# Kernel optimization log

Measured on AMD Instinct MI355X. Metric: run time of the kernel, lower is better.

Reference implementation:

```python
import jax, jax.numpy as jnp
import numpy as np

H = 256          # NUM_HIDDEN_NODES
D = 2 * H        # encoder feature dim
C_CLS = 1000     # NUM_CLASSES
B = 16
S = 1024
STEPS = 8
WINDOW = 4
MIN_VAL = 1e-8   # min_val global in original


def moving_sum(x, back, fwd):
    # x: [B, T]; sum over window [i-back, i+fwd] (zero padded), as conv1d with ones kernel
    xp = jnp.pad(x, ((0, 0), (back, fwd)))
    k = jnp.ones((1, 1, back + fwd + 1), x.dtype)
    y = jax.lax.conv_general_dilated(xp[:, None, :], k, window_strides=(1,),
                                     padding='VALID', dimension_numbers=('NCH', 'OIH', 'NCH'))
    return y[:, 0, :]


def setup_inputs() -> dict:
    key = jax.random.key(0)
    ks = jax.random.split(key, 24)
    def lin(k, i, o):
        return jax.random.normal(k, (i, o), jnp.float32) * np.float32(1.0 / np.sqrt(i))
    def vec(k, n):
        return jax.random.normal(k, (n,), jnp.float32) * np.float32(1.0 / np.sqrt(n))
    return {
        'enc_output': jax.random.normal(ks[0], (B, S, D), jnp.float32),
        'target': jax.random.randint(ks[1], (B, STEPS), 0, C_CLS),
        'length_enc': jax.random.randint(ks[2], (B,), S // 2, S + 1),
        'noise': jax.random.normal(ks[3], (STEPS, B, S), jnp.float32),
        'Ws_mono_w': lin(ks[4], H, D), 'Ws_mono_b': jnp.zeros((D,), jnp.float32),
        'Wh_mono': lin(ks[5], D, D),
        'v_mono': vec(ks[6], D),
        'g_mono': jnp.full((1,), 1.0 / np.sqrt(D), jnp.float32),
        'r_mono': jnp.full((1,), -4.0, jnp.float32),
        'Ws_chunk_w': lin(ks[7], H, D), 'Ws_chunk_b': jnp.zeros((D,), jnp.float32),
        'Wh_chunk': lin(ks[8], D, D),
        'v_chunk': vec(ks[9], D),
        'L_sy': lin(ks[10], H, H),
        'L_gy_w': lin(ks[11], D, H), 'L_gy_b': jnp.zeros((H,), jnp.float32),
        'L_yy_w': lin(ks[12], H, C_CLS), 'L_yy_b': jnp.zeros((C_CLS,), jnp.float32),
        'L_ys': jax.random.normal(ks[13], (C_CLS, 4 * H), jnp.float32) * 0.02,
        'L_ss': lin(ks[14], H, 4 * H),
        'L_gs_w': lin(ks[15], D, 4 * H), 'L_gs_b': jnp.zeros((4 * H,), jnp.float32),
    }


def reference(enc_output, target, length_enc, noise,
              Ws_mono_w, Ws_mono_b, Wh_mono, v_mono, g_mono, r_mono,
              Ws_chunk_w, Ws_chunk_b, Wh_chunk, v_chunk,
              L_sy, L_gy_w, L_gy_b, L_yy_w, L_yy_b, L_ys, L_ss, L_gs_w, L_gs_b):
    Bn, Sn, _ = enc_output.shape
    Hn = L_sy.shape[0]
    mask = jnp.arange(Sn)[None, :] >= length_enc[:, None]   # True = padded
    neg_inf = jnp.float32(-jnp.inf)
    # step-invariant encoder projections (hoisted out of decode loop)
    enc_mono = enc_output @ Wh_mono     # [B,S,D]
    enc_chunk = enc_output @ Wh_chunk   # [B,S,D]
    v_norm = g_mono[0] / jnp.linalg.norm(v_mono)

    def step(carry, xs):
        s, c, a_prev = carry
        nz, tgt = xs
        # monotonic energies
        tmp1 = jnp.tanh(enc_mono + (s @ Ws_mono_w + Ws_mono_b)[:, None, :])
        e_mono = jnp.einsum('bsd,d->bs', v_norm * tmp1, v_mono) + r_mono[0]
        e_mono = jnp.where(mask, neg_inf, e_mono)
        p = jax.nn.sigmoid(e_mono + nz)
        # monotonic attention recurrence via stable cumsum/cumprod
        logf = jnp.log(jnp.clip(1.0 - p[:, :-1], MIN_VAL, 1.0))
        cpp = jnp.concatenate([jnp.ones((Bn, 1), p.dtype), jnp.exp(jnp.cumsum(logf, axis=1))], axis=1)
        q = cpp * jnp.cumsum(a_prev / jnp.clip(cpp, MIN_VAL, 1.0), axis=1)
        alpha = jnp.clip(p * q, MIN_VAL, 1.0)
        # chunkwise attention
        tmp2 = jnp.tanh(enc_chunk + (s @ Ws_chunk_w + Ws_chunk_b)[:, None, :])
        e_ch = jnp.where(mask, neg_inf, jnp.einsum('bsd,d->bs', tmp2, v_chunk))
        e_ch = e_ch - jnp.max(e_ch, axis=1, keepdims=True)
        ex = jnp.clip(jnp.exp(e_ch), 1e-5, None)
        denom = jnp.clip(moving_sum(ex, WINDOW - 1, 0), 1e-10, None)
        beta = ex * moving_sum(alpha / denom, 0, WINDOW - 1)
        ctx = jnp.einsum('bs,bsd->bd', beta, enc_output)
        # decoder LSTM cell
        rec = L_ys[tgt] + s @ L_ss + ctx @ L_gs_w + L_gs_b
        i, f, g, o = jnp.split(rec, 4, axis=1)
        c_new = jax.nn.sigmoid(f) * c + jax.nn.sigmoid(i) * jnp.tanh(g)
        s_new = jax.nn.sigmoid(o) * jnp.tanh(c_new)
        y = jnp.tanh(ctx @ L_gy_w + L_gy_b + s_new @ L_sy) @ L_yy_w + L_yy_b
        return (s_new, c_new, jax.lax.stop_gradient(alpha)), y

    a0 = jnp.zeros((Bn, Sn), enc_output.dtype).at[:, 0].set(1.0)
    s0 = jnp.zeros((Bn, Hn), enc_output.dtype)
    c0 = jnp.zeros((Bn, Hn), enc_output.dtype)
    _, ys = jax.lax.scan(step, (s0, c0, a0), (noise, target.T))
    return jnp.transpose(ys, (1, 0, 2))   # [B, steps, NUM_CLASSES]
```

## Files before the change

kernel.cpp:

```cpp
#include <hip/hip_runtime.h>
#include <math.h>
#include <float.h>

#define HN 256
#define DN 512
#define CCLS 1000
#define BB 16
#define SS 1024
#define NSTEPS 8
#define G4 1024
#define KV 768

using f16x8 = __attribute__((ext_vector_type(8))) _Float16;
using f32x4 = __attribute__((ext_vector_type(4))) float;

__device__ __forceinline__ void gload_lds16(const void* g, void* l) {
    __builtin_amdgcn_global_load_lds((const __attribute__((address_space(1))) void*)g,
                                     (__attribute__((address_space(3))) void*)l, 16, 0, 0);
}

__device__ __forceinline__ float ftanh(float x) {
    float e = __expf(2.f * x);
    return 1.f - 2.f / (e + 1.f);
}
__device__ __forceinline__ float fsigm(float x) {
    return 1.f / (1.f + __expf(-x));
}

__global__ __launch_bounds__(512) void init_k(const float* __restrict__ vM, const float* __restrict__ g,
                                              const float* __restrict__ Wsmb, const float* __restrict__ Wscb,
                                              float* __restrict__ aA, float* __restrict__ sA,
                                              float* __restrict__ cbuf,
                                              float* __restrict__ smb, float* __restrict__ scb,
                                              float* __restrict__ vn) {
    int bid = blockIdx.x, t = threadIdx.x;
    if (bid == 80) {
        __shared__ float red[512];
        float x = vM[t];
        red[t] = x * x;
        __syncthreads();
        for (int off = 256; off > 0; off >>= 1) {
            if (t < off) red[t] += red[t + off];
            __syncthreads();
        }
        if (t == 0) vn[0] = g[0] / sqrtf(red[0]);
        return;
    }
    int i = bid * 512 + t;
    if (i < 16384) {
        aA[i] = ((i & (SS - 1)) == 0) ? 1.f : 0.f;
    } else if (i < 20480) {
        sA[i - 16384] = 0.f;
    } else if (i < 24576) {
        cbuf[i - 20480] = 0.f;
    } else if (i < 32768) {
        int j = i - 24576;
        smb[j] = Wsmb[j & (DN - 1)];
    } else {
        int j = i - 32768;
        scb[j] = Wscb[j & (DN - 1)];
    }
}

__global__ __launch_bounds__(256) void conv_enc_k(const float* __restrict__ in,
                                                  _Float16* __restrict__ out) {
    size_t i = ((size_t)blockIdx.x * 256 + threadIdx.x) * 8;
    float4 a = *(const float4*)(in + i);
    float4 b = *(const float4*)(in + i + 4);
    f16x8 o;
    o[0] = (_Float16)a.x; o[1] = (_Float16)a.y; o[2] = (_Float16)a.z; o[3] = (_Float16)a.w;
    o[4] = (_Float16)b.x; o[5] = (_Float16)b.y; o[6] = (_Float16)b.z; o[7] = (_Float16)b.w;
    *(f16x8*)(out + i) = o;
}

__global__ __launch_bounds__(256) void convW_k(const float* __restrict__ W1,
                                               const float* __restrict__ W2,
                                               _Float16* __restrict__ WcT) {
    int kt = blockIdx.x;
    int nt = blockIdx.y;
    __shared__ _Float16 tile[32][33];
    int tx = threadIdx.x & 31, ty = threadIdx.x >> 5;
    int n0 = nt * 32, k0 = kt * 32;
    for (int r = 0; r < 32; r += 8) {
        int k = k0 + ty + r, n = n0 + tx;
        float v = (n < 512) ? W1[(size_t)k * 512 + n] : W2[(size_t)k * 512 + (n - 512)];
        tile[tx][ty + r] = (_Float16)v;
    }
    __syncthreads();
    for (int r = 0; r < 32; r += 8) {
        int n = n0 + ty + r, k = k0 + tx;
        WcT[(size_t)n * 512 + k] = tile[ty + r][tx];
    }
}

__global__ __launch_bounds__(256) void transAll_k(const float* __restrict__ Lss, const float* __restrict__ Lgs,
                                                  const float* __restrict__ Lsy, const float* __restrict__ Lgy,
                                                  const float* __restrict__ Wsm, const float* __restrict__ Wsc,
                                                  const float* __restrict__ Lyy,
                                                  float* __restrict__ WgT, float* __restrict__ WyT,
                                                  float* __restrict__ WpT, float* __restrict__ LyyT) {
    int bid = blockIdx.x;
    const float* src; float* dst; int R, C, dstride, coloff, ctiles;
    if (bid < 256)       { src = Lss; dst = WgT;  R = 256; C = 1024; dstride = KV; coloff = 0;  ctiles = 32; }
    else if (bid < 768)  { src = Lgs; dst = WgT;  R = 512; C = 1024; dstride = KV; coloff = HN; ctiles = 32; bid -= 256; }
    else if (bid < 832)  { src = Lsy; dst = WyT;  R = 256; C = 256;  dstride = KV; coloff = 0;  ctiles = 8;  bid -= 768; }
    else if (bid < 960)  { src = Lgy; dst = WyT;  R = 512; C = 256;  dstride = KV; coloff = HN; ctiles = 8;  bid -= 832; }
    else if (bid < 1088) { src = Wsm; dst = WpT;  R = 256; C = 512;  dstride = HN; coloff = 0;  ctiles = 16; bid -= 960; }
    else if (bid < 1216) { src = Wsc; dst = WpT + (size_t)DN * HN; R = 256; C = 512; dstride = HN; coloff = 0; ctiles = 16; bid -= 1088; }
    else                 { src = Lyy; dst = LyyT; R = 256; C = 1000; dstride = HN; coloff = 0;  ctiles = 32; bid -= 1216; }
    int ct = bid % ctiles, rt = bid / ctiles;
    __shared__ float tile[32][33];
    int c0 = ct * 32, r0 = rt * 32;
    int tx = threadIdx.x & 31, ty = threadIdx.x >> 5;
    for (int rr = 0; rr < 32; rr += 8) {
        int r = r0 + ty + rr, cc = c0 + tx;
        tile[ty + rr][tx] = (r < R && cc < C) ? src[(size_t)r * C + cc] : 0.f;
    }
    __syncthreads();
    for (int rr = 0; rr < 32; rr += 8) {
        int cc = c0 + ty + rr, r = r0 + tx;
        if (cc < C && r < R) dst[(size_t)cc * dstride + coloff + r] = tile[tx][ty + rr];
    }
}

__global__ __launch_bounds__(256) void gemm16_k(const _Float16* __restrict__ A16,
                                                const _Float16* __restrict__ WcT,
                                                _Float16* __restrict__ encMC) {
    __shared__ _Float16 Alds[128 * 32];
    __shared__ _Float16 Blds[128 * 32];
    int bm = blockIdx.x;
    int bn = blockIdx.y;
    int tid = threadIdx.x;
    int lane = tid & 63;
    int w = tid >> 6;
    int wr = w >> 1, wc = w & 1;
    int lr = lane & 15;
    int kg = lane >> 4;
    f32x4 acc[4][4];
#pragma unroll
    for (int i = 0; i < 4; i++)
#pragma unroll
        for (int j = 0; j < 4; j++) acc[i][j] = (f32x4){0.f, 0.f, 0.f, 0.f};
    int wavebase = tid & ~63;
    for (int k0 = 0; k0 < 512; k0 += 32) {
        __syncthreads();
#pragma unroll
        for (int is = 0; is < 2; is++) {
            int l = is * 256 + tid;
            int row = l >> 2, kgs = l & 3;
            int kp = kgs ^ ((row ^ (row >> 2)) & 3);
            gload_lds16(A16 + (size_t)(bm * 128 + row) * 512 + k0 + kp * 8,
                        (char*)Alds + (size_t)(is * 256 + wavebase) * 16);
            gload_lds16(WcT + (size_t)(bn * 128 + row) * 512 + k0 + kp * 8,
                        (char*)Blds + (size_t)(is * 256 + wavebase) * 16);
        }
        __syncthreads();
        f16x8 af[4], bf[4];
#pragma unroll
        for (int mi = 0; mi < 4; mi++) {
            int r = wr * 64 + mi * 16 + lr;
            int kp = kg ^ ((r ^ (r >> 2)) & 3);
            af[mi] = *(const f16x8*)(Alds + r * 32 + kp * 8);
        }
#pragma unroll
        for (int ni = 0; ni < 4; ni++) {
            int cgl = wc * 64 + ni * 16 + lr;
            int kp = kg ^ ((cgl ^ (cgl >> 2)) & 3);
            bf[ni] = *(const f16x8*)(Blds + cgl * 32 + kp * 8);
        }
#pragma unroll
        for (int mi = 0; mi < 4; mi++)
#pragma unroll
            for (int ni = 0; ni < 4; ni++)
                acc[mi][ni] = __builtin_amdgcn_mfma_f32_16x16x32_f16(af[mi], bf[ni], acc[mi][ni], 0, 0, 0);
    }
    int cr = lane >> 4;
#pragma unroll
    for (int mi = 0; mi < 4; mi++)
#pragma unroll
        for (int ni = 0; ni < 4; ni++) {
            int col = bn * 128 + wc * 64 + ni * 16 + lr;
#pragma unroll
            for (int j = 0; j < 4; j++) {
                int row = bm * 128 + wr * 64 + mi * 16 + cr * 4 + j;
                encMC[(size_t)row * 1024 + col] = (_Float16)acc[mi][ni][j];
            }
        }
}

__device__ __forceinline__ void out_proj(int bid2, int tid, float* shbuf,
                                         const float* __restrict__ yv,
                                         const float* __restrict__ LyyT, const float* __restrict__ Lyyb,
                                         float* __restrict__ out, int tt) {
    for (int i = tid * 4; i < BB * HN; i += 1024)
        *(float4*)&shbuf[i] = *(const float4*)&yv[i];
    __syncthreads();
    int wave = tid >> 6, lane = tid & 63;
    int c0 = (bid2 * 4 + wave) * 4;
    for (int q = 0; q < 4; q++) {
        int cc = c0 + q;
        if (cc >= CCLS) break;
        const float* wp = LyyT + (size_t)cc * HN;
        float acc[BB] = {0.f};
#pragma unroll
        for (int k = 0; k < 4; k++) {
            int e = lane + k * 64;
            float wv = wp[e];
#pragma unroll
            for (int b = 0; b < BB; b++) acc[b] = fmaf(wv, shbuf[b * HN + e], acc[b]);
        }
#pragma unroll
        for (int b = 0; b < BB; b++)
#pragma unroll
            for (int off = 32; off > 0; off >>= 1) acc[b] += __shfl_xor(acc[b], off);
        if (lane == 0) {
            float bias = Lyyb[cc];
#pragma unroll
            for (int b = 0; b < BB; b++) out[((size_t)b * NSTEPS + tt) * CCLS + cc] = acc[b] + bias;
        }
    }
}

__global__ __launch_bounds__(256) void energy_out_k(const _Float16* __restrict__ encMC,
                                                    const float* __restrict__ sm, const float* __restrict__ sc,
                                                    const float* __restrict__ vM, const float* __restrict__ vC,
                                                    const float* __restrict__ vnorm, const float* __restrict__ rmono,
                                                    const int* __restrict__ len, const float* __restrict__ noise_t,
                                                    float* __restrict__ p, float* __restrict__ ech,
                                                    const float* __restrict__ yv,
                                                    const float* __restrict__ LyyT, const float* __restrict__ Lyyb,
                                                    float* __restrict__ out, int t) {
    __shared__ float shbuf[BB * HN];
    int tid = threadIdx.x;
    if (blockIdx.x >= 4096) {
        if (t > 0) out_proj(blockIdx.x - 4096, tid, shbuf, yv, LyyT, Lyyb, out, t - 1);
        return;
    }
    int wave = blockIdx.x * 4 + (tid >> 6);
    int lane = tid & 63;
    int b = wave >> 10;
    int si = wave & 1023;
    const f16x8* row = (const f16x8*)(encMC + (size_t)wave * 1024);
    f16x8 em = row[lane];
    f16x8 ec = row[64 + lane];
    int d0 = lane * 8;
    float4 sma = *(const float4*)&sm[b * DN + d0];
    float4 smbv = *(const float4*)&sm[b * DN + d0 + 4];
    float4 sca = *(const float4*)&sc[b * DN + d0];
    float4 scbv = *(const float4*)&sc[b * DN + d0 + 4];
    float4 vma = *(const float4*)&vM[d0];
    float4 vmb = *(const float4*)&vM[d0 + 4];
    float4 vca = *(const float4*)&vC[d0];
    float4 vcb = *(const float4*)&vC[d0 + 4];
    float smv[8] = {sma.x, sma.y, sma.z, sma.w, smbv.x, smbv.y, smbv.z, smbv.w};
    float scv[8] = {sca.x, sca.y, sca.z, sca.w, scbv.x, scbv.y, scbv.z, scbv.w};
    float vmv[8] = {vma.x, vma.y, vma.z, vma.w, vmb.x, vmb.y, vmb.z, vmb.w};
    float vcv[8] = {vca.x, vca.y, vca.z, vca.w, vcb.x, vcb.y, vcb.z, vcb.w};
    float s1 = 0.f, s2 = 0.f;
#pragma unroll
    for (int j = 0; j < 8; j++) {
        s1 += ftanh((float)em[j] + smv[j]) * vmv[j];
        s2 += ftanh((float)ec[j] + scv[j]) * vcv[j];
    }
#pragma unroll
    for (int off = 32; off > 0; off >>= 1) {
        s1 += __shfl_xor(s1, off);
        s2 += __shfl_xor(s2, off);
    }
    if (lane == 0) {
        bool masked = (si >= len[b]);
        float pe = 0.f;
        if (!masked) pe = fsigm(vnorm[0] * s1 + rmono[0] + noise_t[b * SS + si]);
        p[b * SS + si] = pe;
        ech[b * SS + si] = masked ? -INFINITY : s2;
    }
}

__global__ __launch_bounds__(64) void scan_k(const float* __restrict__ p,
                                             const float* __restrict__ aprev,
                                             const float* __restrict__ ech,
                                             float* __restrict__ anew,
                                             float* __restrict__ beta) {
    int b = blockIdx.x;
    int l = threadIdx.x;
    int base = b * SS + l * 16;
    float pv[16], ap[16], eh[16];
#pragma unroll
    for (int k = 0; k < 16; k += 4) {
        *(float4*)&pv[k] = *(const float4*)&p[base + k];
        *(float4*)&ap[k] = *(const float4*)&aprev[base + k];
        *(float4*)&eh[k] = *(const float4*)&ech[base + k];
    }
    float ls[16];
    float run = 0.f;
#pragma unroll
    for (int k = 0; k < 16; k++) {
        float lf = __logf(fminf(fmaxf(1.f - pv[k], 1e-8f), 1.f));
        if (l == 63 && k == 15) lf = 0.f;
        run += lf;
        ls[k] = run;
    }
    float incl = run;
#pragma unroll
    for (int off = 1; off < 64; off <<= 1) {
        float n = __shfl_up(incl, off);
        if (l >= off) incl += n;
    }
    float basew = incl - run;
    float cpp[16];
#pragma unroll
    for (int k = 0; k < 16; k++)
        cpp[k] = __expf(basew + (k ? ls[k - 1] : 0.f));
    float us[16];
    float run2 = 0.f;
#pragma unroll
    for (int k = 0; k < 16; k++) {
        run2 += ap[k] / fminf(fmaxf(cpp[k], 1e-8f), 1.f);
        us[k] = run2;
    }
    float incl2 = run2;
#pragma unroll
    for (int off = 1; off < 64; off <<= 1) {
        float n = __shfl_up(incl2, off);
        if (l >= off) incl2 += n;
    }
    float basew2 = incl2 - run2;
    float al[16];
#pragma unroll
    for (int k = 0; k < 16; k++)
        al[k] = fminf(fmaxf(pv[k] * (cpp[k] * (basew2 + us[k])), 1e-8f), 1.f);
#pragma unroll
    for (int k = 0; k < 16; k += 4)
        *(float4*)&anew[base + k] = *(float4*)&al[k];
    float mx = eh[0];
#pragma unroll
    for (int k = 1; k < 16; k++) mx = fmaxf(mx, eh[k]);
#pragma unroll
    for (int off = 32; off > 0; off >>= 1) mx = fmaxf(mx, __shfl_xor(mx, off));
    float ex[16];
#pragma unroll
    for (int k = 0; k < 16; k++) ex[k] = fmaxf(__expf(eh[k] - mx), 1e-5f);
    float exm1 = __shfl_up(ex[15], 1); if (l == 0) exm1 = 0.f;
    float exm2 = __shfl_up(ex[14], 1); if (l == 0) exm2 = 0.f;
    float exm3 = __shfl_up(ex[13], 1); if (l == 0) exm3 = 0.f;
    float r[16];
    {
        float d0 = ex[0] + exm1 + exm2 + exm3;
        float d1 = ex[1] + ex[0] + exm1 + exm2;
        float d2 = ex[2] + ex[1] + ex[0] + exm1;
        r[0] = al[0] / fmaxf(d0, 1e-10f);
        r[1] = al[1] / fmaxf(d1, 1e-10f);
        r[2] = al[2] / fmaxf(d2, 1e-10f);
    }
#pragma unroll
    for (int k = 3; k < 16; k++)
        r[k] = al[k] / fmaxf(ex[k] + ex[k - 1] + ex[k - 2] + ex[k - 3], 1e-10f);
    float rp1 = __shfl_down(r[0], 1); if (l == 63) rp1 = 0.f;
    float rp2 = __shfl_down(r[1], 1); if (l == 63) rp2 = 0.f;
    float rp3 = __shfl_down(r[2], 1); if (l == 63) rp3 = 0.f;
    float bt[16];
#pragma unroll
    for (int k = 0; k < 13; k++)
        bt[k] = ex[k] * (r[k] + r[k + 1] + r[k + 2] + r[k + 3]);
    bt[13] = ex[13] * (r[13] + r[14] + r[15] + rp1);
    bt[14] = ex[14] * (r[14] + r[15] + rp1 + rp2);
    bt[15] = ex[15] * (r[15] + rp1 + rp2 + rp3);
#pragma unroll
    for (int k = 0; k < 16; k += 4)
        *(float4*)&beta[base + k] = *(float4*)&bt[k];
}

__global__ __launch_bounds__(512) void ctxpart_k(const float* __restrict__ beta,
                                                 const _Float16* __restrict__ enc16,
                                                 float* __restrict__ part8) {
    __shared__ float red[8][DN];
    int b = blockIdx.x, ch = blockIdx.y;
    int tid = threadIdx.x, wv = tid >> 6, lane = tid & 63;
    int s0 = ch * 128;
    float acc[8] = {0.f};
    const _Float16* ebase = enc16 + ((size_t)(b * SS + s0)) * DN + lane * 8;
    const float* bp = beta + b * SS + s0;
#pragma unroll 4
    for (int rr = 0; rr < 16; rr++) {
        int s = wv + rr * 8;
        float bv = bp[s];
        f16x8 ld = *(const f16x8*)(ebase + (size_t)s * DN);
#pragma unroll
        for (int j = 0; j < 8; j++) acc[j] = fmaf(bv, (float)ld[j], acc[j]);
    }
#pragma unroll
    for (int j = 0; j < 8; j++) red[wv][lane * 8 + j] = acc[j];
    __syncthreads();
    float s = 0.f;
#pragma unroll
    for (int wq = 0; wq < 8; wq++) s += red[wq][tid];
    part8[((size_t)(b * 8 + ch)) * DN + tid] = s;
}

__global__ __launch_bounds__(512) void gl_k(const float* __restrict__ part8,
                                            const float* __restrict__ sIn,
                                            const float* __restrict__ WgT,
                                            const int* __restrict__ target, int t,
                                            const float* __restrict__ Lys, const float* __restrict__ Lgsb,
                                            float* __restrict__ c, float* __restrict__ sOut,
                                            float* __restrict__ ctxbuf) {
    __shared__ float xl[BB * KV];
    __shared__ float recL[16][BB];
    int tid = threadIdx.x;
    for (int i = tid; i < BB * HN; i += 512)
        xl[(i >> 8) * KV + (i & (HN - 1))] = sIn[i];
    for (int i = tid; i < BB * DN; i += 512) {
        int bb = i >> 9, d = i & (DN - 1);
        const float* pp = part8 + (size_t)bb * (8 * DN) + d;
        float v = ((pp[0] + pp[DN]) + (pp[2 * DN] + pp[3 * DN])) +
                  ((pp[4 * DN] + pp[5 * DN]) + (pp[6 * DN] + pp[7 * DN]));
        xl[bb * KV + HN + d] = v;
        if (blockIdx.x == 0) ctxbuf[i] = v;
    }
    __syncthreads();
    int wv = tid >> 6, lane = tid & 63;
    int h0 = blockIdx.x * 4;
    int ri0 = wv * 2, ri1 = ri0 + 1;
    const float* w0p = WgT + (size_t)((ri0 >> 2) * HN + h0 + (ri0 & 3)) * KV;
    const float* w1p = WgT + (size_t)((ri1 >> 2) * HN + h0 + (ri1 & 3)) * KV;
    float acc0[BB] = {0.f}, acc1[BB] = {0.f};
#pragma unroll
    for (int j = 0; j < 12; j++) {
        int e = lane + j * 64;
        float w0 = w0p[e], w1 = w1p[e];
#pragma unroll
        for (int b = 0; b < BB; b++) {
            float xv = xl[b * KV + e];
            acc0[b] = fmaf(w0, xv, acc0[b]);
            acc1[b] = fmaf(w1, xv, acc1[b]);
        }
    }
#pragma unroll
    for (int b = 0; b < BB; b++)
#pragma unroll
        for (int off = 32; off > 0; off >>= 1) {
            acc0[b] += __shfl_xor(acc0[b], off);
            acc1[b] += __shfl_xor(acc1[b], off);
        }
    if (lane == 0) {
#pragma unroll
        for (int b = 0; b < BB; b++) {
            recL[ri0][b] = acc0[b];
            recL[ri1][b] = acc1[b];
        }
    }
    __syncthreads();
    if (tid < 64) {
        int b = tid & 15, hh = tid >> 4;
        int h = h0 + hh;
        int tgt = target[b * NSTEPS + t];
        const float* ys = Lys + (size_t)tgt * G4;
        float ri = recL[0 * 4 + hh][b] + ys[h] + Lgsb[h];
        float rf = recL[1 * 4 + hh][b] + ys[h + HN] + Lgsb[h + HN];
        float rg = recL[2 * 4 + hh][b] + ys[h + 2 * HN] + Lgsb[h + 2 * HN];
        float ro = recL[3 * 4 + hh][b] + ys[h + 3 * HN] + Lgsb[h + 3 * HN];
        float cn = fsigm(rf) * c[b * HN + h] + fsigm(ri) * ftanh(rg);
        float sn = fsigm(ro) * ftanh(cn);
        c[b * HN + h] = cn;
        sOut[b * HN + h] = sn;
    }
}

__global__ __launch_bounds__(256) void ypj_k(const float* __restrict__ sNew,
                                             const float* __restrict__ ctxbuf,
                                             const float* __restrict__ WyT, const float* __restrict__ Lgyb,
                                             const float* __restrict__ WpT,
                                             const float* __restrict__ Wsmb, const float* __restrict__ Wscb,
                                             float* __restrict__ yv,
                                             float* __restrict__ smb, float* __restrict__ scb) {
    __shared__ float sl[BB * KV];
    int tid = threadIdx.x;
    for (int i = tid; i < BB * HN; i += 256)
        sl[(i >> 8) * KV + (i & (HN - 1))] = sNew[i];
    for (int i = tid; i < BB * DN; i += 256)
        sl[(i >> 9) * KV + HN + (i & (DN - 1))] = ctxbuf[i];
    __syncthreads();
    int wave = tid >> 6, lane = tid & 63;
    if (blockIdx.x < 16) {
        int h0 = blockIdx.x * 16 + wave * 4;
        for (int q = 0; q < 4; q++) {
            int h = h0 + q;
            const float* wp = WyT + (size_t)h * KV;
            float acc[BB] = {0.f};
#pragma unroll
            for (int j = 0; j < 12; j++) {
                int e = lane + j * 64;
                float wv = wp[e];
#pragma unroll
                for (int b = 0; b < BB; b++) acc[b] = fmaf(wv, sl[b * KV + e], acc[b]);
            }
#pragma unroll
            for (int b = 0; b < BB; b++)
#pragma unroll
                for (int off = 32; off > 0; off >>= 1) acc[b] += __shfl_xor(acc[b], off);
            if (lane == 0) {
#pragma unroll
                for (int b = 0; b < BB; b++) yv[b * HN + h] = ftanh(acc[b] + Lgyb[h]);
            }
        }
    } else {
        int j0 = (blockIdx.x - 16) * 16 + wave * 4;
        for (int q = 0; q < 4; q++) {
            int jc = j0 + q;
            const float* wp = WpT + (size_t)jc * HN;
            float acc[BB] = {0.f};
#pragma unroll
            for (int k = 0; k < 4; k++) {
                int e = lane + k * 64;
                float wv = wp[e];
#pragma unroll
                for (int b = 0; b < BB; b++) acc[b] = fmaf(wv, sl[b * KV + e], acc[b]);
            }
#pragma unroll
            for (int b = 0; b < BB; b++)
#pragma unroll
                for (int off = 32; off > 0; off >>= 1) acc[b] += __shfl_xor(acc[b], off);
            if (lane == 0) {
                if (jc < DN) {
#pragma unroll
                    for (int b = 0; b < BB; b++) smb[b * DN + jc] = acc[b] + Wsmb[jc];
                } else {
                    int jj = jc - DN;
#pragma unroll
                    for (int b = 0; b < BB; b++) scb[b * DN + jj] = acc[b] + Wscb[jj];
                }
            }
        }
    }
}

__global__ __launch_bounds__(256) void out_k(const float* __restrict__ yv,
                                             const float* __restrict__ LyyT, const float* __restrict__ Lyyb,
                                             float* __restrict__ out, int t) {
    __shared__ float shbuf[BB * HN];
    out_proj(blockIdx.x, threadIdx.x, shbuf, yv, LyyT, Lyyb, out, t);
}

extern "C" void kernel_launch(void* const* d_in, const int* in_sizes, int n_in,
                              void* d_out, int out_size, void* d_ws, size_t ws_size,
                              hipStream_t stream) {
    const float* enc  = (const float*)d_in[0];
    const int*   target = (const int*)d_in[1];
    const int*   len  = (const int*)d_in[2];
    const float* noise = (const float*)d_in[3];
    const float* Wsm  = (const float*)d_in[4];
    const float* Wsmb = (const float*)d_in[5];
    const float* WhM  = (const float*)d_in[6];
    const float* vM   = (const float*)d_in[7];
    const float* g    = (const float*)d_in[8];
    const float* rm   = (const float*)d_in[9];
    const float* Wsc  = (const float*)d_in[10];
    const float* Wscb = (const float*)d_in[11];
    const float* WhC  = (const float*)d_in[12];
    const float* vC   = (const float*)d_in[13];
    const float* Lsy  = (const float*)d_in[14];
    const float* Lgy  = (const float*)d_in[15];
    const float* Lgyb = (const float*)d_in[16];
    const float* Lyy  = (const float*)d_in[17];
    const float* Lyyb = (const float*)d_in[18];
    const float* Lys  = (const float*)d_in[19];
    const float* Lss  = (const float*)d_in[20];
    const float* Lgs  = (const float*)d_in[21];
    const float* Lgsb = (const float*)d_in[22];
    float* out = (float*)d_out;

    char* w = (char*)d_ws;
    size_t off = 0;
    auto alloc = [&](size_t bytes) { void* pp = w + off; off += (bytes + 255) & ~(size_t)255; return pp; };
    _Float16* A16   = (_Float16*)alloc((size_t)BB * SS * DN * 2);
    _Float16* WcT   = (_Float16*)alloc((size_t)1024 * 512 * 2);
    _Float16* encMC = (_Float16*)alloc((size_t)BB * SS * 1024 * 2);
    float* WgT  = (float*)alloc((size_t)G4 * KV * 4);
    float* WyT  = (float*)alloc((size_t)HN * KV * 4);
    float* WpT  = (float*)alloc((size_t)G4 * HN * 4);
    float* LyyT = (float*)alloc((size_t)CCLS * HN * 4);
    float* smb   = (float*)alloc(BB * DN * 4);
    float* scb   = (float*)alloc(BB * DN * 4);
    float* pbuf  = (float*)alloc(BB * SS * 4);
    float* ech   = (float*)alloc(BB * SS * 4);
    float* aA    = (float*)alloc(BB * SS * 4);
    float* aBf   = (float*)alloc(BB * SS * 4);
    float* betab = (float*)alloc(BB * SS * 4);
    float* part8 = (float*)alloc((size_t)BB * 8 * DN * 4);
    float* ctxbuf = (float*)alloc((size_t)BB * DN * 4);
    float* sA    = (float*)alloc((size_t)BB * HN * 4);
    float* sB    = (float*)alloc((size_t)BB * HN * 4);
    float* yvb   = (float*)alloc((size_t)BB * HN * 4);
    float* cbuf  = (float*)alloc(BB * HN * 4);
    float* vn    = (float*)alloc(16);
    (void)ws_size; (void)in_sizes; (void)n_in; (void)out_size;

    init_k<<<81, 512, 0, stream>>>(vM, g, Wsmb, Wscb, aA, sA, cbuf, smb, scb, vn);
    conv_enc_k<<<4096, 256, 0, stream>>>(enc, A16);
    convW_k<<<dim3(16, 32), 256, 0, stream>>>(WhM, WhC, WcT);
    gemm16_k<<<dim3(128, 8), 256, 0, stream>>>(A16, WcT, encMC);
    transAll_k<<<1472, 256, 0, stream>>>(Lss, Lgs, Lsy, Lgy, Wsm, Wsc, Lyy, WgT, WyT, WpT, LyyT);

    for (int t = 0; t < NSTEPS; t++) {
        float* ain  = (t % 2 == 0) ? aA : aBf;
        float* aout = (t % 2 == 0) ? aBf : aA;
        float* sIn  = (t % 2 == 0) ? sA : sB;
        float* sOut = (t % 2 == 0) ? sB : sA;
        energy_out_k<<<4159, 256, 0, stream>>>(encMC, smb, scb, vM, vC, vn, rm,
                                               len, noise + (size_t)t * BB * SS, pbuf, ech,
                                               yvb, LyyT, Lyyb, out, t);
        scan_k<<<BB, 64, 0, stream>>>(pbuf, ain, ech, aout, betab);
        ctxpart_k<<<dim3(BB, 8), 512, 0, stream>>>(betab, A16, part8);
        gl_k<<<64, 512, 0, stream>>>(part8, sIn, WgT, target, t, Lys, Lgsb, cbuf, sOut, ctxbuf);
        ypj_k<<<80, 256, 0, stream>>>(sOut, ctxbuf, WyT, Lgyb, WpT, Wsmb, Wscb, yvb, smb, scb);
    }
    out_k<<<63, 256, 0, stream>>>(yvb, LyyT, Lyyb, out, NSTEPS - 1);
}
```

Baseline: 529.5 us.

## Fuse prep kernels, fuse scan into ctx partials, skip masked energy rows

Merges the init, encoder conversion, weight conversion and transpose kernels into one prep launch. Fuses the per-batch monotonic scan into the context-partial kernel: each of the 8 chunk blocks recomputes the scan redundantly and keeps beta in shared memory, which removes one launch per step and the beta round trip through global memory. The energy kernel now has each wave handle 8 positions and skips whole groups beyond the sequence length, cutting encMC reads for padded positions. The costs are 8x redundant scan work and fewer, larger energy blocks, which may lower occupancy.

```diff
diff --git a/kernel.cpp b/kernel.cpp
--- a/kernel.cpp
+++ b/kernel.cpp
@@ -27,100 +27,101 @@
     return 1.f / (1.f + __expf(-x));
 }
 
-__global__ __launch_bounds__(512) void init_k(const float* __restrict__ vM, const float* __restrict__ g,
+__global__ __launch_bounds__(256) void prep_k(const float* __restrict__ enc,
+                                              const float* __restrict__ W1, const float* __restrict__ W2,
+                                              const float* __restrict__ Lss, const float* __restrict__ Lgs,
+                                              const float* __restrict__ Lsy, const float* __restrict__ Lgy,
+                                              const float* __restrict__ Wsm, const float* __restrict__ Wsc,
+                                              const float* __restrict__ Lyy,
+                                              const float* __restrict__ vM, const float* __restrict__ g,
                                               const float* __restrict__ Wsmb, const float* __restrict__ Wscb,
+                                              _Float16* __restrict__ A16, _Float16* __restrict__ WcT,
+                                              float* __restrict__ WgT, float* __restrict__ WyT,
+                                              float* __restrict__ WpT, float* __restrict__ LyyT,
                                               float* __restrict__ aA, float* __restrict__ sA,
                                               float* __restrict__ cbuf,
                                               float* __restrict__ smb, float* __restrict__ scb,
                                               float* __restrict__ vn) {
-    int bid = blockIdx.x, t = threadIdx.x;
-    if (bid == 80) {
-        __shared__ float red[512];
-        float x = vM[t];
-        red[t] = x * x;
+    int bid = blockIdx.x, tid = threadIdx.x;
+    if (bid < 4096) {
+        size_t i = ((size_t)bid * 256 + tid) * 8;
+        float4 a = *(const float4*)(enc + i);
+        float4 b = *(const float4*)(enc + i + 4);
+        f16x8 o;
+        o[0] = (_Float16)a.x; o[1] = (_Float16)a.y; o[2] = (_Float16)a.z; o[3] = (_Float16)a.w;
+        o[4] = (_Float16)b.x; o[5] = (_Float16)b.y; o[6] = (_Float16)b.z; o[7] = (_Float16)b.w;
+        *(f16x8*)(A16 + i) = o;
+        return;
+    }
+    if (bid < 4608) {
+        int x = bid - 4096;
+        int kt = x & 15, nt = x >> 4;
+        __shared__ _Float16 tile[32][33];
+        int tx = tid & 31, ty = tid >> 5;
+        int n0 = nt * 32, k0 = kt * 32;
+        for (int r = 0; r < 32; r += 8) {
+            int k = k0 + ty + r, n = n0 + tx;
+            float v = (n < 512) ? W1[(size_t)k * 512 + n] : W2[(size_t)k * 512 + (n - 512)];
+            tile[tx][ty + r] = (_Float16)v;
+        }
         __syncthreads();
-        for (int off = 256; off > 0; off >>= 1) {
-            if (t < off) red[t] += red[t + off];
-            __syncthreads();
-        }
-        if (t == 0) vn[0] = g[0] / sqrtf(red[0]);
+        for (int r = 0; r < 32; r += 8) {
+            int n = n0 + ty + r, k = k0 + tx;
+            WcT[(size_t)n * 512 + k] = tile[ty + r][tx];
+        }
         return;
     }
-    int i = bid * 512 + t;
-    if (i < 16384) {
-        aA[i] = ((i & (SS - 1)) == 0) ? 1.f : 0.f;
-    } else if (i < 20480) {
-        sA[i - 16384] = 0.f;
-    } else if (i < 24576) {
-        cbuf[i - 20480] = 0.f;
-    } else if (i < 32768) {
-        int j = i - 24576;
-        smb[j] = Wsmb[j & (DN - 1)];
-    } else {
-        int j = i - 32768;
-        scb[j] = Wscb[j & (DN - 1)];
-    }
-}
-
-__global__ __launch_bounds__(256) void conv_enc_k(const float* __restrict__ in,
-                                                  _Float16* __restrict__ out) {
-    size_t i = ((size_t)blockIdx.x * 256 + threadIdx.x) * 8;
-    float4 a = *(const float4*)(in + i);
-    float4 b = *(const float4*)(in + i + 4);
-    f16x8 o;
-    o[0] = (_Float16)a.x; o[1] = (_Float16)a.y; o[2] = (_Float16)a.z; o[3] = (_Float16)a.w;
-    o[4] = (_Float16)b.x; o[5] = (_Float16)b.y; o[6] = (_Float16)b.z; o[7] = (_Float16)b.w;
-    *(f16x8*)(out + i) = o;
-}
-
-__global__ __launch_bounds__(256) void convW_k(const float* __restrict__ W1,
-                                               const float* __restrict__ W2,
-                                               _Float16* __restrict__ WcT) {
-    int kt = blockIdx.x;
-    int nt = blockIdx.y;
-    __shared__ _Float16 tile[32][33];
-    int tx = threadIdx.x & 31, ty = threadIdx.x >> 5;
-    int n0 = nt * 32, k0 = kt * 32;
-    for (int r = 0; r < 32; r += 8) {
-        int k = k0 + ty + r, n = n0 + tx;
-        float v = (n < 512) ? W1[(size_t)k * 512 + n] : W2[(size_t)k * 512 + (n - 512)];
-        tile[tx][ty + r] = (_Float16)v;
-    }
+    if (bid < 6080) {
+        int b2 = bid - 4608;
+        const float* src; float* dst; int R, C, dstride, coloff, ctiles;
+        if (b2 < 256)       { src = Lss; dst = WgT;  R = 256; C = 1024; dstride = KV; coloff = 0;  ctiles = 32; }
+        else if (b2 < 768)  { src = Lgs; dst = WgT;  R = 512; C = 1024; dstride = KV; coloff = HN; ctiles = 32; b2 -= 256; }
+        else if (b2 < 832)  { src = Lsy; dst = WyT;  R = 256; C = 256;  dstride = KV; coloff = 0;  ctiles = 8;  b2 -= 768; }
+        else if (b2 < 960)  { src = Lgy; dst = WyT;  R = 512; C = 256;  dstride = KV; coloff = HN; ctiles = 8;  b2 -= 832; }
+        else if (b2 < 1088) { src = Wsm; dst = WpT;  R = 256; C = 512;  dstride = HN; coloff = 0;  ctiles = 16; b2 -= 960; }
+        else if (b2 < 1216) { src = Wsc; dst = WpT + (size_t)DN * HN; R = 256; C = 512; dstride = HN; coloff = 0; ctiles = 16; b2 -= 1088; }
+        else                { src = Lyy; dst = LyyT; R = 256; C = 1000; dstride = HN; coloff = 0;  ctiles = 32; b2 -= 1216; }
+        int ct = b2 % ctiles, rt = b2 / ctiles;
+        __shared__ float ftile[32][33];
+        int c0 = ct * 32, r0 = rt * 32;
+        int tx = tid & 31, ty = tid >> 5;
+        for (int rr = 0; rr < 32; rr += 8) {
+            int r = r0 + ty + rr, cc = c0 + tx;
+            ftile[ty + rr][tx] = (r < R && cc < C) ? src[(size_t)r * C + cc] : 0.f;
+        }
+        __syncthreads();
+        for (int rr = 0; rr < 32; rr += 8) {
+            int cc = c0 + ty + rr, r = r0 + tx;
+            if (cc < C && r < R) dst[(size_t)cc * dstride + coloff + r] = ftile[tx][ty + rr];
+        }
+        return;
+    }
+    if (bid < 6240) {
+        int i = (bid - 6080) * 256 + tid;
+        if (i < 16384) {
+            aA[i] = ((i & (SS - 1)) == 0) ? 1.f : 0.f;
+        } else if (i < 20480) {
+            sA[i - 16384] = 0.f;
+        } else if (i < 24576) {
+            cbuf[i - 20480] = 0.f;
+        } else if (i < 32768) {
+            int j = i - 24576;
+            smb[j] = Wsmb[j & (DN - 1)];
+        } else {
+            int j = i - 32768;
+            scb[j] = Wscb[j & (DN - 1)];
+        }
+        return;
+    }
+    __shared__ float red[256];
+    float x0 = vM[tid], x1 = vM[tid + 256];
+    red[tid] = x0 * x0 + x1 * x1;
     __syncthreads();
-    for (int r = 0; r < 32; r += 8) {
-        int n = n0 + ty + r, k = k0 + tx;
-        WcT[(size_t)n * 512 + k] = tile[ty + r][tx];
-    }
-}
-
-__global__ __launch_bounds__(256) void transAll_k(const float* __restrict__ Lss, const float* __restrict__ Lgs,
-                                                  const float* __restrict__ Lsy, const float* __restrict__ Lgy,
-                                                  const float* __restrict__ Wsm, const float* __restrict__ Wsc,
-                                                  const float* __restrict__ Lyy,
-                                                  float* __restrict__ WgT, float* __restrict__ WyT,
-                                                  float* __restrict__ WpT, float* __restrict__ LyyT) {
-    int bid = blockIdx.x;
-    const float* src; float* dst; int R, C, dstride, coloff, ctiles;
-    if (bid < 256)       { src = Lss; dst = WgT;  R = 256; C = 1024; dstride = KV; coloff = 0;  ctiles = 32; }
-    else if (bid < 768)  { src = Lgs; dst = WgT;  R = 512; C = 1024; dstride = KV; coloff = HN; ctiles = 32; bid -= 256; }
-    else if (bid < 832)  { src = Lsy; dst = WyT;  R = 256; C = 256;  dstride = KV; coloff = 0;  ctiles = 8;  bid -= 768; }
-    else if (bid < 960)  { src = Lgy; dst = WyT;  R = 512; C = 256;  dstride = KV; coloff = HN; ctiles = 8;  bid -= 832; }
-    else if (bid < 1088) { src = Wsm; dst = WpT;  R = 256; C = 512;  dstride = HN; coloff = 0;  ctiles = 16; bid -= 960; }
-    else if (bid < 1216) { src = Wsc; dst = WpT + (size_t)DN * HN; R = 256; C = 512; dstride = HN; coloff = 0; ctiles = 16; bid -= 1088; }
-    else                 { src = Lyy; dst = LyyT; R = 256; C = 1000; dstride = HN; coloff = 0;  ctiles = 32; bid -= 1216; }
-    int ct = bid % ctiles, rt = bid / ctiles;
-    __shared__ float tile[32][33];
-    int c0 = ct * 32, r0 = rt * 32;
-    int tx = threadIdx.x & 31, ty = threadIdx.x >> 5;
-    for (int rr = 0; rr < 32; rr += 8) {
-        int r = r0 + ty + rr, cc = c0 + tx;
-        tile[ty + rr][tx] = (r < R && cc < C) ? src[(size_t)r * C + cc] : 0.f;
-    }
-    __syncthreads();
-    for (int rr = 0; rr < 32; rr += 8) {
-        int cc = c0 + ty + rr, r = r0 + tx;
-        if (cc < C && r < R) dst[(size_t)cc * dstride + coloff + r] = tile[tx][ty + rr];
-    }
+    for (int off = 128; off > 0; off >>= 1) {
+        if (tid < off) red[tid] += red[tid + off];
+        __syncthreads();
+    }
+    if (tid == 0) vn[0] = g[0] / sqrtf(red[0]);
 }
 
 __global__ __launch_bounds__(256) void gemm16_k(const _Float16* __restrict__ A16,
@@ -232,17 +233,24 @@
                                                     float* __restrict__ out, int t) {
     __shared__ float shbuf[BB * HN];
     int tid = threadIdx.x;
-    if (blockIdx.x >= 4096) {
-        if (t > 0) out_proj(blockIdx.x - 4096, tid, shbuf, yv, LyyT, Lyyb, out, t - 1);
+    if (blockIdx.x >= 512) {
+        if (t > 0) out_proj(blockIdx.x - 512, tid, shbuf, yv, LyyT, Lyyb, out, t - 1);
         return;
     }
-    int wave = blockIdx.x * 4 + (tid >> 6);
-    int lane = tid & 63;
-    int b = wave >> 10;
-    int si = wave & 1023;
-    const f16x8* row = (const f16x8*)(encMC + (size_t)wave * 1024);
-    f16x8 em = row[lane];
-    f16x8 ec = row[64 + lane];
+    int wv = tid >> 6, lane = tid & 63;
+    int b = blockIdx.x >> 5;
+    int lenb = len[b];
+    int si0 = (blockIdx.x & 31) * 32 + wv * 8;
+    if (si0 >= lenb) {
+        if (lane == 0) {
+#pragma unroll
+            for (int k = 0; k < 8; k++) {
+                p[b * SS + si0 + k] = 0.f;
+                ech[b * SS + si0 + k] = -INFINITY;
+            }
+        }
+        return;
+    }
     int d0 = lane * 8;
     float4 sma = *(const float4*)&sm[b * DN + d0];
     float4 smbv = *(const float4*)&sm[b * DN + d0 + 4];
@@ -256,130 +264,144 @@
     float scv[8] = {sca.x, sca.y, sca.z, sca.w, scbv.x, scbv.y, scbv.z, scbv.w};
     float vmv[8] = {vma.x, vma.y, vma.z, vma.w, vmb.x, vmb.y, vmb.z, vmb.w};
     float vcv[8] = {vca.x, vca.y, vca.z, vca.w, vcb.x, vcb.y, vcb.z, vcb.w};
-    float s1 = 0.f, s2 = 0.f;
-#pragma unroll
-    for (int j = 0; j < 8; j++) {
-        s1 += ftanh((float)em[j] + smv[j]) * vmv[j];
-        s2 += ftanh((float)ec[j] + scv[j]) * vcv[j];
-    }
-#pragma unroll
-    for (int off = 32; off > 0; off >>= 1) {
-        s1 += __shfl_xor(s1, off);
-        s2 += __shfl_xor(s2, off);
-    }
-    if (lane == 0) {
-        bool masked = (si >= len[b]);
-        float pe = 0.f;
-        if (!masked) pe = fsigm(vnorm[0] * s1 + rmono[0] + noise_t[b * SS + si]);
-        p[b * SS + si] = pe;
-        ech[b * SS + si] = masked ? -INFINITY : s2;
-    }
-}
-
-__global__ __launch_bounds__(64) void scan_k(const float* __restrict__ p,
-                                             const float* __restrict__ aprev,
-                                             const float* __restrict__ ech,
-                                             float* __restrict__ anew,
-                                             float* __restrict__ beta) {
-    int b = blockIdx.x;
-    int l = threadIdx.x;
-    int base = b * SS + l * 16;
-    float pv[16], ap[16], eh[16];
-#pragma unroll
-    for (int k = 0; k < 16; k += 4) {
-        *(float4*)&pv[k] = *(const float4*)&p[base + k];
-        *(float4*)&ap[k] = *(const float4*)&aprev[base + k];
-        *(float4*)&eh[k] = *(const float4*)&ech[base + k];
-    }
-    float ls[16];
-    float run = 0.f;
-#pragma unroll
-    for (int k = 0; k < 16; k++) {
-        float lf = __logf(fminf(fmaxf(1.f - pv[k], 1e-8f), 1.f));
-        if (l == 63 && k == 15) lf = 0.f;
-        run += lf;
-        ls[k] = run;
-    }
-    float incl = run;
-#pragma unroll
-    for (int off = 1; off < 64; off <<= 1) {
-        float n = __shfl_up(incl, off);
-        if (l >= off) incl += n;
-    }
-    float basew = incl - run;
-    float cpp[16];
-#pragma unroll
-    for (int k = 0; k < 16; k++)
-        cpp[k] = __expf(basew + (k ? ls[k - 1] : 0.f));
-    float us[16];
-    float run2 = 0.f;
-#pragma unroll
-    for (int k = 0; k < 16; k++) {
-        run2 += ap[k] / fminf(fmaxf(cpp[k], 1e-8f), 1.f);
-        us[k] = run2;
-    }
-    float incl2 = run2;
-#pragma unroll
-    for (int off = 1; off < 64; off <<= 1) {
-        float n = __shfl_up(incl2, off);
-        if (l >= off) incl2 += n;
-    }
-    float basew2 = incl2 - run2;
-    float al[16];
-#pragma unroll
-    for (int k = 0; k < 16; k++)
-        al[k] = fminf(fmaxf(pv[k] * (cpp[k] * (basew2 + us[k])), 1e-8f), 1.f);
-#pragma unroll
-    for (int k = 0; k < 16; k += 4)
-        *(float4*)&anew[base + k] = *(float4*)&al[k];
-    float mx = eh[0];
-#pragma unroll
-    for (int k = 1; k < 16; k++) mx = fmaxf(mx, eh[k]);
-#pragma unroll
-    for (int off = 32; off > 0; off >>= 1) mx = fmaxf(mx, __shfl_xor(mx, off));
-    float ex[16];
-#pragma unroll
-    for (int k = 0; k < 16; k++) ex[k] = fmaxf(__expf(eh[k] - mx), 1e-5f);
-    float exm1 = __shfl_up(ex[15], 1); if (l == 0) exm1 = 0.f;
-    float exm2 = __shfl_up(ex[14], 1); if (l == 0) exm2 = 0.f;
-    float exm3 = __shfl_up(ex[13], 1); if (l == 0) exm3 = 0.f;
-    float r[16];
-    {
-        float d0 = ex[0] + exm1 + exm2 + exm3;
-        float d1 = ex[1] + ex[0] + exm1 + exm2;
-        float d2 = ex[2] + ex[1] + ex[0] + exm1;
-        r[0] = al[0] / fmaxf(d0, 1e-10f);
-        r[1] = al[1] / fmaxf(d1, 1e-10f);
-        r[2] = al[2] / fmaxf(d2, 1e-10f);
-    }
-#pragma unroll
-    for (int k = 3; k < 16; k++)
-        r[k] = al[k] / fmaxf(ex[k] + ex[k - 1] + ex[k - 2] + ex[k - 3], 1e-10f);
-    float rp1 = __shfl_down(r[0], 1); if (l == 63) rp1 = 0.f;
-    float rp2 = __shfl_down(r[1], 1); if (l == 63) rp2 = 0.f;
-    float rp3 = __shfl_down(r[2], 1); if (l == 63) rp3 = 0.f;
-    float bt[16];
-#pragma unroll
-    for (int k = 0; k < 13; k++)
-        bt[k] = ex[k] * (r[k] + r[k + 1] + r[k + 2] + r[k + 3]);
-    bt[13] = ex[13] * (r[13] + r[14] + r[15] + rp1);
-    bt[14] = ex[14] * (r[14] + r[15] + rp1 + rp2);
-    bt[15] = ex[15] * (r[15] + rp1 + rp2 + rp3);
-#pragma unroll
-    for (int k = 0; k < 16; k += 4)
-        *(float4*)&beta[base + k] = *(float4*)&bt[k];
-}
-
-__global__ __launch_bounds__(512) void ctxpart_k(const float* __restrict__ beta,
+    float vnv = vnorm[0], rmv = rmono[0];
+    const float* nz = noise_t + b * SS;
+#pragma unroll
+    for (int k = 0; k < 8; k++) {
+        int si = si0 + k;
+        if (si >= lenb) {
+            if (lane == 0) {
+                p[b * SS + si] = 0.f;
+                ech[b * SS + si] = -INFINITY;
+            }
+            continue;
+        }
+        const f16x8* row = (const f16x8*)(encMC + ((size_t)b * SS + si) * 1024);
+        f16x8 em = row[lane];
+        f16x8 ec = row[64 + lane];
+        float s1 = 0.f, s2 = 0.f;
+#pragma unroll
+        for (int j = 0; j < 8; j++) {
+            s1 += ftanh((float)em[j] + smv[j]) * vmv[j];
+            s2 += ftanh((float)ec[j] + scv[j]) * vcv[j];
+        }
+#pragma unroll
+        for (int off = 32; off > 0; off >>= 1) {
+            s1 += __shfl_xor(s1, off);
+            s2 += __shfl_xor(s2, off);
+        }
+        if (lane == 0) {
+            p[b * SS + si] = fsigm(vnv * s1 + rmv + nz[si]);
+            ech[b * SS + si] = s2;
+        }
+    }
+}
+
+__global__ __launch_bounds__(512) void scanctx_k(const float* __restrict__ p,
+                                                 const float* __restrict__ aprev,
+                                                 const float* __restrict__ ech,
                                                  const _Float16* __restrict__ enc16,
+                                                 float* __restrict__ anew,
                                                  float* __restrict__ part8) {
+    __shared__ float betaL[SS];
     __shared__ float red[8][DN];
     int b = blockIdx.x, ch = blockIdx.y;
-    int tid = threadIdx.x, wv = tid >> 6, lane = tid & 63;
+    int tid = threadIdx.x;
+    if (tid < 64) {
+        int l = tid;
+        int base = b * SS + l * 16;
+        float pv[16], ap[16], eh[16];
+#pragma unroll
+        for (int k = 0; k < 16; k += 4) {
+            *(float4*)&pv[k] = *(const float4*)&p[base + k];
+            *(float4*)&ap[k] = *(const float4*)&aprev[base + k];
+            *(float4*)&eh[k] = *(const float4*)&ech[base + k];
+        }
+        float ls[16];
+        float run = 0.f;
+#pragma unroll
+        for (int k = 0; k < 16; k++) {
+            float lf = __logf(fminf(fmaxf(1.f - pv[k], 1e-8f), 1.f));
+            if (l == 63 && k == 15) lf = 0.f;
+            run += lf;
+            ls[k] = run;
+        }
+        float incl = run;
+#pragma unroll
+        for (int off = 1; off < 64; off <<= 1) {
+            float n = __shfl_up(incl, off);
+            if (l >= off) incl += n;
+        }
+        float basew = incl - run;
+        float cpp[16];
+#pragma unroll
+        for (int k = 0; k < 16; k++)
+            cpp[k] = __expf(basew + (k ? ls[k - 1] : 0.f));
+        float us[16];
+        float run2 = 0.f;
+#pragma unroll
+        for (int k = 0; k < 16; k++) {
+            run2 += ap[k] / fminf(fmaxf(cpp[k], 1e-8f), 1.f);
+            us[k] = run2;
+        }
+        float incl2 = run2;
+#pragma unroll
+        for (int off = 1; off < 64; off <<= 1) {
+            float n = __shfl_up(incl2, off);
+            if (l >= off) incl2 += n;
+        }
+        float basew2 = incl2 - run2;
+        float al[16];
+#pragma unroll
+        for (int k = 0; k < 16; k++)
+            al[k] = fminf(fmaxf(pv[k] * (cpp[k] * (basew2 + us[k])), 1e-8f), 1.f);
+        if (ch == 0) {
+#pragma unroll
+            for (int k = 0; k < 16; k += 4)
+                *(float4*)&anew[base + k] = *(float4*)&al[k];
+        }
+        float mx = eh[0];
+#pragma unroll
+        for (int k = 1; k < 16; k++) mx = fmaxf(mx, eh[k]);
+#pragma unroll
+        for (int off = 32; off > 0; off >>= 1) mx = fmaxf(mx, __shfl_xor(mx, off));
+        float ex[16];
+#pragma unroll
+        for (int k = 0; k < 16; k++) ex[k] = fmaxf(__expf(eh[k] - mx), 1e-5f);
+        float exm1 = __shfl_up(ex[15], 1); if (l == 0) exm1 = 0.f;
+        float exm2 = __shfl_up(ex[14], 1); if (l == 0) exm2 = 0.f;
+        float exm3 = __shfl_up(ex[13], 1); if (l == 0) exm3 = 0.f;
+        float r[16];
+        {
+            float dd0 = ex[0] + exm1 + exm2 + exm3;
+            float dd1 = ex[1] + ex[0] + exm1 + exm2;
+            float dd2 = ex[2] + ex[1] + ex[0] + exm1;
+            r[0] = al[0] / fmaxf(dd0, 1e-10f);
+            r[1] = al[1] / fmaxf(dd1, 1e-10f);
+            r[2] = al[2] / fmaxf(dd2, 1e-10f);
+        }
+#pragma unroll
+        for (int k = 3; k < 16; k++)
+            r[k] = al[k] / fmaxf(ex[k] + ex[k - 1] + ex[k - 2] + ex[k - 3], 1e-10f);
+        float rp1 = __shfl_down(r[0], 1); if (l == 63) rp1 = 0.f;
+        float rp2 = __shfl_down(r[1], 1); if (l == 63) rp2 = 0.f;
+        float rp3 = __shfl_down(r[2], 1); if (l == 63) rp3 = 0.f;
+        float bt[16];
+#pragma unroll
+        for (int k = 0; k < 13; k++)
+            bt[k] = ex[k] * (r[k] + r[k + 1] + r[k + 2] + r[k + 3]);
+        bt[13] = ex[13] * (r[13] + r[14] + r[15] + rp1);
+        bt[14] = ex[14] * (r[14] + r[15] + rp1 + rp2);
+        bt[15] = ex[15] * (r[15] + rp1 + rp2 + rp3);
+#pragma unroll
+        for (int k = 0; k < 16; k++) betaL[l * 16 + k] = bt[k];
+    }
+    __syncthreads();
+    int wv = tid >> 6, lane = tid & 63;
     int s0 = ch * 128;
     float acc[8] = {0.f};
     const _Float16* ebase = enc16 + ((size_t)(b * SS + s0)) * DN + lane * 8;
-    const float* bp = beta + b * SS + s0;
+    const float* bp = betaL + s0;
 #pragma unroll 4
     for (int rr = 0; rr < 16; rr++) {
         int s = wv + rr * 8;
@@ -585,7 +607,6 @@
     float* ech   = (float*)alloc(BB * SS * 4);
     float* aA    = (float*)alloc(BB * SS * 4);
     float* aBf   = (float*)alloc(BB * SS * 4);
-    float* betab = (float*)alloc(BB * SS * 4);
     float* part8 = (float*)alloc((size_t)BB * 8 * DN * 4);
     float* ctxbuf = (float*)alloc((size_t)BB * DN * 4);
     float* sA    = (float*)alloc((size_t)BB * HN * 4);
@@ -595,22 +616,21 @@
     float* vn    = (float*)alloc(16);
     (void)ws_size; (void)in_sizes; (void)n_in; (void)out_size;
 
-    init_k<<<81, 512, 0, stream>>>(vM, g, Wsmb, Wscb, aA, sA, cbuf, smb, scb, vn);
-    conv_enc_k<<<4096, 256, 0, stream>>>(enc, A16);
-    convW_k<<<dim3(16, 32), 256, 0, stream>>>(WhM, WhC, WcT);
+    prep_k<<<6241, 256, 0, stream>>>(enc, WhM, WhC, Lss, Lgs, Lsy, Lgy, Wsm, Wsc, Lyy,
+                                     vM, g, Wsmb, Wscb,
+                                     A16, WcT, WgT, WyT, WpT, LyyT,
+                                     aA, sA, cbuf, smb, scb, vn);
     gemm16_k<<<dim3(128, 8), 256, 0, stream>>>(A16, WcT, encMC);
-    transAll_k<<<1472, 256, 0, stream>>>(Lss, Lgs, Lsy, Lgy, Wsm, Wsc, Lyy, WgT, WyT, WpT, LyyT);
 
     for (int t = 0; t < NSTEPS; t++) {
         float* ain  = (t % 2 == 0) ? aA : aBf;
         float* aout = (t % 2 == 0) ? aBf : aA;
         float* sIn  = (t % 2 == 0) ? sA : sB;
         float* sOut = (t % 2 == 0) ? sB : sA;
-        energy_out_k<<<4159, 256, 0, stream>>>(encMC, smb, scb, vM, vC, vn, rm,
-                                               len, noise + (size_t)t * BB * SS, pbuf, ech,
-                                               yvb, LyyT, Lyyb, out, t);
-        scan_k<<<BB, 64, 0, stream>>>(pbuf, ain, ech, aout, betab);
-        ctxpart_k<<<dim3(BB, 8), 512, 0, stream>>>(betab, A16, part8);
+        energy_out_k<<<575, 256, 0, stream>>>(encMC, smb, scb, vM, vC, vn, rm,
+                                              len, noise + (size_t)t * BB * SS, pbuf, ech,
+                                              yvb, LyyT, Lyyb, out, t);
+        scanctx_k<<<dim3(BB, 8), 512, 0, stream>>>(pbuf, ain, ech, A16, aout, part8);
         gl_k<<<64, 512, 0, stream>>>(part8, sIn, WgT, target, t, Lys, Lgsb, cbuf, sOut, ctxbuf);
         ypj_k<<<80, 256, 0, stream>>>(sOut, ctxbuf, WyT, Lgyb, WpT, Wsmb, Wscb, yvb, smb, scb);
     }
```

Result: faster. 489.9 us (-7.5%).
